# Optimization experiments

Measured on AMD Instinct MI355X. Metric: run time of the kernel, lower is better.

## Reference

```python
import jax, jax.numpy as jnp
import numpy as np

B, T, D = 64, 32, 64          # batch, timesteps, input_dim (= output_dim)
N, V, R, H = 1024, 64, 4, 512  # locations, vec_size, read/write pairs, controller_dim
DIN = D + R * V                # controller input dim


def _address(mem, k, beta, g, s, gamma, w_prev):
    # mem: [B,N,V], k: [B,V], beta/g/gamma: [B,1], s: [B,3], w_prev: [B,N]
    beta = jax.nn.softplus(beta)
    g = jax.nn.sigmoid(g)
    s = jax.nn.softmax(s, axis=1)
    gamma = 1.0 + jax.nn.softplus(gamma)
    a = mem + 1e-16
    b = k[:, None, :] + 1e-16
    na = jnp.maximum(jnp.linalg.norm(a, axis=-1), 1e-8)   # [B,N]
    nb = jnp.maximum(jnp.linalg.norm(b, axis=-1), 1e-8)   # [B,1]
    cos = jnp.sum(a * b, axis=-1) / (na * nb)             # [B,N]
    w_c = jax.nn.softmax(beta * cos, axis=1)
    w_g = g * w_c + (1.0 - g) * w_prev
    # circular shift conv, kernel width 3: out[i] = s0*w[i-1] + s1*w[i] + s2*w[i+1]
    w_s = (s[:, 0:1] * jnp.roll(w_g, 1, axis=1)
           + s[:, 1:2] * w_g
           + s[:, 2:3] * jnp.roll(w_g, -1, axis=1))
    w = w_s ** gamma
    return w / (jnp.sum(w, axis=1, keepdims=True) + 1e-16)


def _forward(x, mem_bias, lstm_h_bias, lstm_c_bias, W_ih, W_hh, b_ih, b_hh,
             read_W, read_b, write_W, write_b, read_init, out_W, out_b):
    dt = x.dtype
    mem0 = jnp.broadcast_to(mem_bias, (B, N, V)).astype(dt)
    reads0 = jnp.broadcast_to(read_init[:, None, :], (R, B, V)).astype(dt)
    h0 = jnp.broadcast_to(lstm_h_bias, (B, H)).astype(dt)
    c0 = jnp.broadcast_to(lstm_c_bias, (B, H)).astype(dt)
    ws0 = jnp.zeros((2 * R, B, N), dt)   # per-head previous weights (read_i at 2i, write_i at 2i+1)

    def step(carry, x_t):
        mem, reads, h, c, ws = carry
        contr_x = jnp.concatenate([x_t, reads.transpose(1, 0, 2).reshape(B, R * V)], axis=1)
        # single-layer LSTM cell, pytorch gate order i,f,g,o
        gates = contr_x @ W_ih.T + b_ih + h @ W_hh.T + b_hh
        gi, gf, gg, go = jnp.split(gates, 4, axis=1)
        c_new = jax.nn.sigmoid(gf) * c + jax.nn.sigmoid(gi) * jnp.tanh(gg)
        h_new = jax.nn.sigmoid(go) * jnp.tanh(c_new)
        co = h_new
        new_reads = []
        new_ws = [None] * (2 * R)
        for i in range(R):
            # read head i
            o_r = co @ read_W[i].T + read_b[i]               # [B, V+6]
            w = _address(mem, o_r[:, :V], o_r[:, V:V+1], o_r[:, V+1:V+2],
                         o_r[:, V+2:V+5], o_r[:, V+5:V+6], ws[2 * i])
            new_ws[2 * i] = w
            new_reads.append(jnp.einsum('bn,bnv->bv', w, mem))
            # write head i
            o_w = co @ write_W[i].T + write_b[i]             # [B, 3V+6]
            e = jax.nn.sigmoid(o_w[:, V+6:2*V+6])
            a = o_w[:, 2*V+6:]
            w2 = _address(mem, o_w[:, :V], o_w[:, V:V+1], o_w[:, V+1:V+2],
                          o_w[:, V+2:V+5], o_w[:, V+5:V+6], ws[2 * i + 1])
            new_ws[2 * i + 1] = w2
            mem = mem * (1.0 - w2[:, :, None] * e[:, None, :]) + w2[:, :, None] * a[:, None, :]
        final_x = jnp.concatenate([co] + new_reads, axis=1)
        y = jax.nn.sigmoid(final_x @ out_W.T + out_b)
        return (mem, jnp.stack(new_reads), h_new, c_new, jnp.stack(new_ws)), y

    _, ys = jax.lax.scan(step, (mem0, reads0, h0, c0, ws0), x.transpose(1, 0, 2))
    return ys.transpose(1, 0, 2)   # [B,T,D]


def setup_inputs() -> dict:
    key = jax.random.key(0)
    ks = jax.random.split(key, 13)
    u = lambda k, shape, s: jax.random.uniform(k, shape, jnp.float32, -s, s)
    s_mem = 1.0 / float(np.sqrt(N + V))
    s_ctl = 5.0 / float(np.sqrt(DIN + H))
    return {
        'x': jax.random.normal(ks[0], (B, T, D), jnp.float32),
        'mem_bias': u(ks[1], (N, V), s_mem),
        'lstm_h_bias': jax.random.normal(ks[2], (1, H), jnp.float32) * 0.05,
        'lstm_c_bias': jax.random.normal(ks[3], (1, H), jnp.float32) * 0.05,
        'W_ih': u(ks[4], (4 * H, DIN), s_ctl),
        'W_hh': u(ks[5], (4 * H, H), s_ctl),
        'b_ih': jnp.zeros((4 * H,), jnp.float32),
        'b_hh': jnp.zeros((4 * H,), jnp.float32),
        'read_W': u(ks[6], (R, V + 6, H), 0.05),
        'read_b': jax.random.normal(ks[7], (R, V + 6), jnp.float32) * 0.01,
        'write_W': u(ks[8], (R, 3 * V + 6, H), 0.05),
        'write_b': jax.random.normal(ks[9], (R, 3 * V + 6), jnp.float32) * 0.01,
        'read_init': jax.random.normal(ks[10], (R, V), jnp.float32) * 0.01,
        'out_W': u(ks[11], (D, H + R * V), 0.05),
        'out_b': jax.random.normal(ks[12], (D,), jnp.float32) * 0.01,
    }


def reference(x, mem_bias, lstm_h_bias, lstm_c_bias, W_ih, W_hh, b_ih, b_hh,
              read_W, read_b, write_W, write_b, read_init, out_W, out_b):
    return _forward(x, mem_bias, lstm_h_bias, lstm_c_bias, W_ih, W_hh, b_ih, b_hh,
                    read_W, read_b, write_W, write_b, read_init, out_W, out_b)
```

## Files before the change

kernel.cpp:

```cpp
#include <hip/hip_runtime.h>
#include <math.h>

#define TT 32
#define DD 64
#define NN 1024
#define VV 64
#define RR 4
#define HH 512

typedef unsigned int uint_t;
typedef unsigned short ushort_t;

__device__ __forceinline__ float sigf(float x) { return 1.0f / (1.0f + __expf(-x)); }
__device__ __forceinline__ float splus(float x) {
  return (x > 0.f) ? (x + log1pf(__expf(-x))) : log1pf(__expf(x));
}
__device__ __forceinline__ ushort_t bfr(float f) {
  uint_t u = __float_as_uint(f);
  return (ushort_t)((u + 0x7fffu + ((u >> 16) & 1u)) >> 16);
}
__device__ __forceinline__ float bflo(uint_t u) { return __uint_as_float(u << 16); }
__device__ __forceinline__ float bfhi(uint_t u) { return __uint_as_float(u & 0xffff0000u); }
__device__ __forceinline__ uint_t packbf(float a, float b) {
  return (uint_t)bfr(a) | ((uint_t)bfr(b) << 16);
}

__global__ void build_gw(const float* __restrict__ W_ih, const float* __restrict__ W_hh,
                         const float* __restrict__ out_W, uint_t* __restrict__ W2g) {
  int idx = blockIdx.x * 256 + threadIdx.x;
  if (idx >= 2112 * 416) return;
  int r = idx / 416, kp = idx - r * 416;
  float v[2];
  #pragma unroll
  for (int q = 0; q < 2; ++q) {
    int k = 2 * kp + q;
    float f;
    if (r < 2048) {
      int h = r >> 2, g = r & 3, row = g * 512 + h;
      f = (k < 320) ? W_ih[(size_t)row * 320 + k] : W_hh[(size_t)row * 512 + (k - 320)];
    } else {
      int j = r - 2048;
      if (k < 64) f = 0.f;
      else if (k < 320) f = out_W[(size_t)j * 768 + 512 + (k - 64)];
      else f = out_W[(size_t)j * 768 + (k - 320)];
    }
    v[q] = f;
  }
  W2g[idx] = packbf(v[0], v[1]);
}
__global__ void build_hw(const float* __restrict__ read_W, const float* __restrict__ write_W,
                         uint_t* __restrict__ W2h) {
  int idx = blockIdx.x * 256 + threadIdx.x;
  if (idx >= 1072 * 256) return;
  int r = idx >> 8, kp = idx & 255;
  const float* src = (r < 280) ? (read_W + (size_t)r * 512) : (write_W + (size_t)(r - 280) * 512);
  W2h[idx] = packbf(src[2 * kp], src[2 * kp + 1]);
}
__global__ void bias_kernel(const float* __restrict__ bi, const float* __restrict__ bh,
                            float* __restrict__ o) {
  int i = blockIdx.x * 256 + threadIdx.x;
  if (i < 2048) o[i] = bi[i] + bh[i];
}
__global__ void k0_init(const float* __restrict__ x, const float* __restrict__ mem_bias,
                        const float* __restrict__ h_bias, const float* __restrict__ c_bias,
                        const float* __restrict__ read_init,
                        ushort_t* __restrict__ g_mem, uint_t* __restrict__ A2,
                        float* __restrict__ g_c, float* __restrict__ g_ws) {
  const int b = blockIdx.x, tid = threadIdx.x;
  {
    const float4* src = (const float4*)(mem_bias + (size_t)tid * VV);
    uint4* dst = (uint4*)(g_mem + (size_t)b * (NN * VV) + (size_t)tid * VV);
    #pragma unroll
    for (int p = 0; p < 8; ++p) {
      float4 va = src[2 * p], vb = src[2 * p + 1];
      uint4 o;
      o.x = packbf(va.x, va.y); o.y = packbf(va.z, va.w);
      o.z = packbf(vb.x, vb.y); o.w = packbf(vb.z, vb.w);
      dst[p] = o;
    }
  }
  if (tid < 416) {
    float v0, v1;
    if (tid < 32)      { v0 = x[((size_t)b * TT) * DD + 2 * tid]; v1 = x[((size_t)b * TT) * DD + 2 * tid + 1]; }
    else if (tid < 160){ int e = 2 * (tid - 32); v0 = read_init[e]; v1 = read_init[e + 1]; }
    else               { int e = 2 * (tid - 160); v0 = h_bias[e]; v1 = h_bias[e + 1]; }
    A2[(size_t)tid * 64 + b] = packbf(v0, v1);
  }
  if (tid < 512) g_c[(size_t)tid * 64 + b] = c_bias[tid];
  for (int i = tid; i < 8192; i += 1024) g_ws[(size_t)b * 8192 + i] = 0.f;
}

__global__ __launch_bounds__(512) void k1s(
    int par, int doGate, int doOut,
    const uint_t* __restrict__ W2g, const uint_t* __restrict__ A2,
    float* __restrict__ g_gp) {
  const int blk = blockIdx.x, tid = threadIdx.x;
  const int lane = tid & 63, u = tid >> 6;
  const bool isGate = (blk < 128);
  if (isGate && !doGate) return;
  if (!isGate && !doOut) return;
  __shared__ uint_t s_tile[52 * 64];
  int kh, hglob = 0, orow = 0;
  size_t wbase;
  if (isGate) {
    int grp = blk >> 1; kh = blk & 1;
    hglob = grp * 8 + u;
    wbase = (size_t)(hglob * 4) * 416;
  } else {
    int ob = blk - 128; kh = ob & 1;
    orow = 2048 + (ob >> 1) * 8 + u;
    wbase = (size_t)orow * 416;
  }
  float acc0 = 0.f, acc1 = 0.f, acc2 = 0.f, acc3 = 0.f;
  for (int cc = 0; cc < 4; ++cc) {
    int c = kh * 4 + cc;
    for (int i = tid; i < 52 * 64; i += 512) {
      int kk = i >> 6, bb = i & 63;
      int kpg = c * 52 + kk;
      int phys = (kpg < 160) ? kpg : kpg + 256 * par;
      s_tile[i] = A2[(size_t)phys * 64 + bb];
    }
    __syncthreads();
    const uint4* w4 = (const uint4*)(W2g + wbase) + c * 13;
    if (isGate) {
      #pragma unroll
      for (int q = 0; q < 13; ++q) {
        uint4 wA = w4[q], wB = w4[104 + q], wC = w4[208 + q], wD = w4[312 + q];
        const uint_t* pA = (const uint_t*)&wA;
        const uint_t* pB = (const uint_t*)&wB;
        const uint_t* pC = (const uint_t*)&wC;
        const uint_t* pD = (const uint_t*)&wD;
        #pragma unroll
        for (int jj = 0; jj < 4; ++jj) {
          uint_t ua = s_tile[(q * 4 + jj) * 64 + lane];
          float a0 = bflo(ua), a1 = bfhi(ua);
          acc0 += bflo(pA[jj]) * a0 + bfhi(pA[jj]) * a1;
          acc1 += bflo(pB[jj]) * a0 + bfhi(pB[jj]) * a1;
          acc2 += bflo(pC[jj]) * a0 + bfhi(pC[jj]) * a1;
          acc3 += bflo(pD[jj]) * a0 + bfhi(pD[jj]) * a1;
        }
      }
    } else {
      #pragma unroll
      for (int q = 0; q < 13; ++q) {
        uint4 wA = w4[q];
        const uint_t* pA = (const uint_t*)&wA;
        #pragma unroll
        for (int jj = 0; jj < 4; ++jj) {
          uint_t ua = s_tile[(q * 4 + jj) * 64 + lane];
          acc0 += bflo(pA[jj]) * bflo(ua) + bfhi(pA[jj]) * bfhi(ua);
        }
      }
    }
    __syncthreads();
  }
  if (isGate) {
    float* d = g_gp + (size_t)(kh * 2112 + hglob * 4) * 64 + lane;
    d[0] = acc0; d[64] = acc1; d[128] = acc2; d[192] = acc3;
  } else {
    g_gp[(size_t)(kh * 2112 + orow) * 64 + lane] = acc0;
  }
}

__global__ __launch_bounds__(512) void k1c(
    int t, int par, int doGate,
    const float* __restrict__ g_gp, const float* __restrict__ gbias,
    uint_t* __restrict__ A2, float* __restrict__ g_c,
    const float* __restrict__ out_b, float* __restrict__ out) {
  const int blk = blockIdx.x, tid = threadIdx.x;
  const int lane = tid & 63, u = tid >> 6;
  if (blk < 64) {
    if (!doGate) return;
    __shared__ float s_h[512];
    const int hglob = blk * 8 + u;
    const float* p0 = g_gp + (size_t)(hglob * 4) * 64 + lane;
    const float* p1 = g_gp + (size_t)(2112 + hglob * 4) * 64 + lane;
    float gi = gbias[hglob]        + p0[0]   + p1[0];
    float gf = gbias[512 + hglob]  + p0[64]  + p1[64];
    float gg = gbias[1024 + hglob] + p0[128] + p1[128];
    float go = gbias[1536 + hglob] + p0[192] + p1[192];
    float c0 = g_c[(size_t)hglob * 64 + lane];
    float cn = sigf(gf) * c0 + sigf(gi) * tanhf(gg);
    float hn = sigf(go) * tanhf(cn);
    g_c[(size_t)hglob * 64 + lane] = cn;
    s_h[u * 64 + lane] = hn;
    __syncthreads();
    if (tid < 256) {
      int q = tid >> 6;
      float h0 = s_h[(2 * q) * 64 + lane], h1 = s_h[(2 * q + 1) * 64 + lane];
      int kp = 160 + 256 * (par ^ 1) + blk * 4 + q;
      A2[(size_t)kp * 64 + lane] = packbf(h0, h1);
    }
  } else {
    if (t == 0) return;
    int j = (blk - 64) * 8 + u;
    float v = out_b[j] + g_gp[(size_t)(2048 + j) * 64 + lane]
                       + g_gp[(size_t)(2112 + 2048 + j) * 64 + lane];
    out[((size_t)lane * TT + (t - 1)) * DD + j] = sigf(v);
  }
}

__global__ __launch_bounds__(512) void k2_heads(
    int wslot, const uint_t* __restrict__ W2h,
    const float* __restrict__ read_b, const float* __restrict__ write_b,
    const uint_t* __restrict__ A2, float* __restrict__ g_headp) {
  const int blk = blockIdx.x, tid = threadIdx.x;
  const int lane = tid & 63, u = tid >> 6;
  const int rgrp = blk >> 1, kh = blk & 1;
  const int r = rgrp * 8 + u;
  __shared__ uint_t s_tile[64 * 64];
  __shared__ float s_tr[8 * 65];
  const int hbase = 160 + 256 * wslot + kh * 128;
  float acc = 0.f;
  const uint_t* wrow = W2h + (size_t)r * 256 + kh * 128;
  for (int c = 0; c < 2; ++c) {
    for (int i = tid; i < 64 * 64; i += 512) {
      int kk = i >> 6, bb = i & 63;
      s_tile[i] = A2[(size_t)(hbase + c * 64 + kk) * 64 + bb];
    }
    __syncthreads();
    #pragma unroll 4
    for (int kk = 0; kk < 64; ++kk) {
      uint_t ua = s_tile[kk * 64 + lane];
      uint_t w = wrow[c * 64 + kk];
      acc += bflo(w) * bflo(ua) + bfhi(w) * bfhi(ua);
    }
    __syncthreads();
  }
  if (kh == 0) acc += (r < 280) ? read_b[r] : write_b[r - 280];
  s_tr[u * 65 + lane] = acc;
  __syncthreads();
  if (tid < 128) {
    int bb = tid & 63, half = tid >> 6;
    float4 v;
    v.x = s_tr[(half * 4 + 0) * 65 + bb];
    v.y = s_tr[(half * 4 + 1) * 65 + bb];
    v.z = s_tr[(half * 4 + 2) * 65 + bb];
    v.w = s_tr[(half * 4 + 3) * 65 + bb];
    *(float4*)(g_headp + (size_t)kh * 69632 + (size_t)bb * 1088 + rgrp * 8 + half * 4) = v;
  }
}

__global__ __launch_bounds__(1024, 4) void k3_mem(
    int t, const float* __restrict__ x, const float* __restrict__ g_headp,
    ushort_t* __restrict__ g_mem, uint_t* __restrict__ A2,
    float* __restrict__ g_ws) {
  const int b = blockIdx.x, tid = threadIdx.x;
  const int lane = tid & 63, wave = tid >> 6;
  extern __shared__ uint_t s_mem[];
  __shared__ alignas(16) float s_wgA[1024];
  __shared__ alignas(16) float s_wgB[1024];
  __shared__ alignas(16) float s_part[1024];
  __shared__ alignas(16) float s_reads[RR * VV];
  __shared__ alignas(16) float s_or[72];
  __shared__ alignas(16) float s_ow[200];
  __shared__ alignas(16) float s_e[VV];
  __shared__ alignas(16) float s_a[VV];
  __shared__ float s_redR[16];
  __shared__ float s_redW[16];
  uint_t* m32 = (uint_t*)(g_mem + (size_t)b * (NN * VV));
  const float* hp = g_headp + (size_t)b * 1088;
  const float* hp1 = hp + 69632;

  float wsr[8];
  #pragma unroll
  for (int s2 = 0; s2 < 8; ++s2) wsr[s2] = g_ws[(size_t)(b * 8 + s2) * 1024 + tid];

  if (tid < 70) s_or[tid] = hp[tid] + hp1[tid];
  else if (tid >= 128 && tid < 326) s_ow[tid - 128] = hp[280 + (tid - 128)] + hp1[280 + (tid - 128)];
  __syncthreads();
  if (tid < VV) { s_e[tid] = sigf(s_ow[70 + tid]); s_a[tid] = s_ow[134 + tid]; }

  for (int hd = 0; hd < RR; ++hd) {
    float dotR = 0.f, dotW = 0.f, nrm2 = 0.f;
    if (hd == 0) {
      const uint4* rowp = (const uint4*)(m32 + (size_t)tid * 32);
      const float4* orf = (const float4*)s_or;
      const float4* owf = (const float4*)s_ow;
      #pragma unroll
      for (int p = 0; p < 8; ++p) {
        uint4 m = rowp[p];
        s_mem[tid * 32 + ((4 * p + 0 + tid) & 31)] = m.x;
        s_mem[tid * 32 + ((4 * p + 1 + tid) & 31)] = m.y;
        s_mem[tid * 32 + ((4 * p + 2 + tid) & 31)] = m.z;
        s_mem[tid * 32 + ((4 * p + 3 + tid) & 31)] = m.w;
        float4 ka = orf[2 * p], kb = orf[2 * p + 1];
        float4 wa = owf[2 * p], wb = owf[2 * p + 1];
        float m0 = bflo(m.x), m1 = bfhi(m.x), m2 = bflo(m.y), m3 = bfhi(m.y);
        float m4 = bflo(m.z), m5 = bfhi(m.z), m6 = bflo(m.w), m7 = bfhi(m.w);
        nrm2 += m0 * m0 + m1 * m1 + m2 * m2 + m3 * m3 + m4 * m4 + m5 * m5 + m6 * m6 + m7 * m7;
        dotR += m0 * ka.x + m1 * ka.y + m2 * ka.z + m3 * ka.w +
                m4 * kb.x + m5 * kb.y + m6 * kb.z + m7 * kb.w;
        dotW += m0 * wa.x + m1 * wa.y + m2 * wa.z + m3 * wa.w +
                m4 * wb.x + m5 * wb.y + m6 * wb.z + m7 * wb.w;
      }
    } else {
      #pragma unroll 8
      for (int c = 0; c < 32; ++c) {
        uint_t u = s_mem[tid * 32 + ((c + tid) & 31)];
        float v0 = bflo(u), v1 = bfhi(u);
        nrm2 += v0 * v0 + v1 * v1;
        dotR += v0 * s_or[2 * c] + v1 * s_or[2 * c + 1];
        dotW += v0 * s_ow[2 * c] + v1 * s_ow[2 * c + 1];
      }
    }
    float kkR, kkW;
    {
      float kR = s_or[lane]; kR *= kR;
      float kW = s_ow[lane]; kW *= kW;
      #pragma unroll
      for (int o = 32; o; o >>= 1) { kR += __shfl_xor(kR, o); kW += __shfl_xor(kW, o); }
      kkR = kR; kkW = kW;
    }
    float na = fmaxf(sqrtf(nrm2), 1e-8f);

    float nbR = fmaxf(sqrtf(kkR), 1e-8f), nbW = fmaxf(sqrtf(kkW), 1e-8f);
    float betaR = splus(s_or[64]), betaW = splus(s_ow[64]);
    float gR = sigf(s_or[65]), gW = sigf(s_ow[65]);
    float r0 = s_or[66], r1 = s_or[67], r2 = s_or[68];
    float q0 = s_ow[66], q1 = s_ow[67], q2 = s_ow[68];
    float mxR = fmaxf(r0, fmaxf(r1, r2)), mxW = fmaxf(q0, fmaxf(q1, q2));
    float eR0 = __expf(r0 - mxR), eR1 = __expf(r1 - mxR), eR2 = __expf(r2 - mxR);
    float eW0 = __expf(q0 - mxW), eW1 = __expf(q1 - mxW), eW2 = __expf(q2 - mxW);
    float siR = 1.0f / (eR0 + eR1 + eR2), siW = 1.0f / (eW0 + eW1 + eW2);
    float gamR = 1.0f + splus(s_or[69]), gamW = 1.0f + splus(s_ow[69]);
    float eeR = __expf(betaR * dotR / (na * nbR));
    float eeW = __expf(betaW * dotW / (na * nbW));
    float vR = eeR, vW = eeW;
    #pragma unroll
    for (int o = 32; o; o >>= 1) { vR += __shfl_xor(vR, o); vW += __shfl_xor(vW, o); }
    if (lane == 0) { s_redR[wave] = vR; s_redW[wave] = vW; }
    __syncthreads();
    float SR = 0.f, SW = 0.f;
    #pragma unroll
    for (int w = 0; w < 16; ++w) { SR += s_redR[w]; SW += s_redW[w]; }
    float wgR = gR * (eeR / SR) + (1.0f - gR) * wsr[2 * hd];
    float wgW = gW * (eeW / SW) + (1.0f - gW) * wsr[2 * hd + 1];
    s_wgA[tid] = wgR;
    s_wgB[tid] = wgW;
    __syncthreads();
    int tm = (tid + 1023) & 1023, tp = (tid + 1) & 1023;
    float wsnR = (eR0 * siR) * s_wgA[tm] + (eR1 * siR) * s_wgA[tid] + (eR2 * siR) * s_wgA[tp];
    float wsnW = (eW0 * siW) * s_wgB[tm] + (eW1 * siW) * s_wgB[tid] + (eW2 * siW) * s_wgB[tp];
    float wpR = __expf(gamR * __logf(wsnR));
    float wpW = __expf(gamW * __logf(wsnW));
    vR = wpR; vW = wpW;
    #pragma unroll
    for (int o = 32; o; o >>= 1) { vR += __shfl_xor(vR, o); vW += __shfl_xor(vW, o); }
    if (lane == 0) { s_redR[wave] = vR; s_redW[wave] = vW; }
    __syncthreads();
    float ZR = 0.f, ZW = 0.f;
    #pragma unroll
    for (int w = 0; w < 16; ++w) { ZR += s_redR[w]; ZW += s_redW[w]; }
    float wRf = wpR / (ZR + 1e-16f);
    float wWf = wpW / (ZW + 1e-16f);
    s_wgA[tid] = wRf;
    s_wgB[tid] = wWf;
    g_ws[(size_t)(b * 8 + 2 * hd) * 1024 + tid] = wRf;
    g_ws[(size_t)(b * 8 + 2 * hd + 1) * 1024 + tid] = wWf;
    __syncthreads();

    if (hd < 3) {
      if (tid < 70) s_or[tid] = hp[(hd + 1) * 70 + tid] + hp1[(hd + 1) * 70 + tid];
      else if (tid >= 128 && tid < 326) {
        int i2 = tid - 128;
        s_ow[i2] = hp[280 + (hd + 1) * 198 + i2] + hp1[280 + (hd + 1) * 198 + i2];
      }
    }

    {
      const int cp = lane & 31, half = lane >> 5;
      const float e0 = s_e[2 * cp], e1 = s_e[2 * cp + 1];
      const float a0 = s_a[2 * cp], a1 = s_a[2 * cp + 1];
      const int rbase = wave * 64 + half;
      float acc0 = 0.f, acc1 = 0.f;
      #pragma unroll 8
      for (int q = 0; q < 32; ++q) {
        int row = rbase + 2 * q;
        int addr = row * 32 + ((cp + row) & 31);
        uint_t uu = s_mem[addr];
        float wRn = s_wgA[row];
        float wWn = s_wgB[row];
        float v0 = bflo(uu), v1 = bfhi(uu);
        acc0 += wRn * v0; acc1 += wRn * v1;
        float n0 = v0 * (1.f - wWn * e0) + wWn * a0;
        float n1 = v1 * (1.f - wWn * e1) + wWn * a1;
        uint_t nu = packbf(n0, n1);
        if (hd < 3) s_mem[addr] = nu;
        else        m32[(size_t)row * 32 + cp] = nu;
      }
      acc0 += __shfl_xor(acc0, 32);
      acc1 += __shfl_xor(acc1, 32);
      if (half == 0) *(float2*)(s_part + wave * 64 + 2 * cp) = make_float2(acc0, acc1);
    }
    __syncthreads();
    if (tid < VV) {
      float s = 0.f;
      #pragma unroll
      for (int w2 = 0; w2 < 16; ++w2) s += s_part[w2 * 64 + tid];
      s_reads[hd * VV + tid] = s;
      if (hd < 3) { s_e[tid] = sigf(s_ow[70 + tid]); s_a[tid] = s_ow[134 + tid]; }
    }
  }
  __syncthreads();

  if (tid < 128)
    A2[(size_t)(32 + tid) * 64 + b] = packbf(s_reads[2 * tid], s_reads[2 * tid + 1]);
  if (tid < 32 && t + 1 < TT) {
    float v0 = x[((size_t)b * TT + t + 1) * DD + 2 * tid];
    float v1 = x[((size_t)b * TT + t + 1) * DD + 2 * tid + 1];
    A2[(size_t)tid * 64 + b] = packbf(v0, v1);
  }
}

extern "C" void kernel_launch(void* const* d_in, const int* in_sizes, int n_in,
                              void* d_out, int out_size, void* d_ws, size_t ws_size,
                              hipStream_t stream) {
  char* ws = (char*)d_ws;
  ushort_t* g_mem = (ushort_t*)ws;
  uint_t* g_A2    = (uint_t*)(ws + 8388608);
  float* g_c      = (float*)(ws + 8560640);
  float* g_ws     = (float*)(ws + 8691712);
  float* g_headp  = (float*)(ws + 10788864);
  uint_t* W2g     = (uint_t*)(ws + 11345920);
  uint_t* W2h     = (uint_t*)(ws + 14860288);
  float* gbias    = (float*)(ws + 15958016);
  float* g_gp     = (float*)(ws + 15966208);

  const float* x        = (const float*)d_in[0];
  const float* mem_bias = (const float*)d_in[1];
  const float* h_bias   = (const float*)d_in[2];
  const float* c_bias   = (const float*)d_in[3];
  const float* W_ih     = (const float*)d_in[4];
  const float* W_hh     = (const float*)d_in[5];
  const float* b_ih     = (const float*)d_in[6];
  const float* b_hh     = (const float*)d_in[7];
  const float* read_W   = (const float*)d_in[8];
  const float* read_b   = (const float*)d_in[9];
  const float* write_W  = (const float*)d_in[10];
  const float* write_b  = (const float*)d_in[11];
  const float* read_init= (const float*)d_in[12];
  const float* out_W    = (const float*)d_in[13];
  const float* out_b    = (const float*)d_in[14];
  float* out = (float*)d_out;

  bias_kernel<<<8, 256, 0, stream>>>(b_ih, b_hh, gbias);
  build_gw<<<3432, 256, 0, stream>>>(W_ih, W_hh, out_W, W2g);
  build_hw<<<1072, 256, 0, stream>>>(read_W, write_W, W2h);
  k0_init<<<64, 1024, 0, stream>>>(x, mem_bias, h_bias, c_bias, read_init,
                                   g_mem, g_A2, g_c, g_ws);
  for (int t = 0; t < TT; ++t) {
    k1s<<<144, 512, 0, stream>>>(t & 1, 1, (t > 0) ? 1 : 0, W2g, g_A2, g_gp);
    k1c<<<72, 512, 0, stream>>>(t, t & 1, 1, g_gp, gbias, g_A2, g_c, out_b, out);
    k2_heads<<<268, 512, 0, stream>>>((t + 1) & 1, W2h, read_b, write_b, g_A2, g_headp);
    k3_mem<<<64, 1024, 131072, stream>>>(t, x, g_headp, g_mem, g_A2, g_ws);
  }
  k1s<<<144, 512, 0, stream>>>(0, 0, 1, W2g, g_A2, g_gp);
  k1c<<<72, 512, 0, stream>>>(TT, 0, 0, g_gp, gbias, g_A2, g_c, out_b, out);
}
```

Before: 3.883 ms.

## Split GEMV K-dimension four ways and defer weight normalization in memory kernel

The gate/output GEMV kernel and the head-projection kernel now split the reduction dimension into four slices instead of two. This doubles the block count (288 and 536 blocks) to fill more compute units on this latency-bound recurrent step, and the consumers sum four partials instead of two. The memory kernel also stores the unnormalized sharpened weights and folds 1/Z into the erase/add vectors and the read result. That removes a block-wide barrier and the normalized-weight writes to shared memory before the memory update. The cost is more partial-sum traffic, a larger workspace, and slightly different rounding from applying the normalization later.

```diff
diff --git a/kernel.cpp b/kernel.cpp
--- a/kernel.cpp
+++ b/kernel.cpp
@@ -96,24 +96,24 @@
     float* __restrict__ g_gp) {
   const int blk = blockIdx.x, tid = threadIdx.x;
   const int lane = tid & 63, u = tid >> 6;
-  const bool isGate = (blk < 128);
+  const bool isGate = (blk < 256);
   if (isGate && !doGate) return;
   if (!isGate && !doOut) return;
   __shared__ uint_t s_tile[52 * 64];
   int kh, hglob = 0, orow = 0;
   size_t wbase;
   if (isGate) {
-    int grp = blk >> 1; kh = blk & 1;
+    int grp = blk >> 2; kh = blk & 3;
     hglob = grp * 8 + u;
     wbase = (size_t)(hglob * 4) * 416;
   } else {
-    int ob = blk - 128; kh = ob & 1;
-    orow = 2048 + (ob >> 1) * 8 + u;
+    int ob = blk - 256; kh = ob & 3;
+    orow = 2048 + (ob >> 2) * 8 + u;
     wbase = (size_t)orow * 416;
   }
   float acc0 = 0.f, acc1 = 0.f, acc2 = 0.f, acc3 = 0.f;
-  for (int cc = 0; cc < 4; ++cc) {
-    int c = kh * 4 + cc;
+  for (int cc = 0; cc < 2; ++cc) {
+    int c = kh * 2 + cc;
     for (int i = tid; i < 52 * 64; i += 512) {
       int kk = i >> 6, bb = i & 63;
       int kpg = c * 52 + kk;
@@ -155,10 +155,10 @@
     __syncthreads();
   }
   if (isGate) {
-    float* d = g_gp + (size_t)(kh * 2112 + hglob * 4) * 64 + lane;
+    float* d = g_gp + (size_t)kh * 135168 + (size_t)(hglob * 4) * 64 + lane;
     d[0] = acc0; d[64] = acc1; d[128] = acc2; d[192] = acc3;
   } else {
-    g_gp[(size_t)(kh * 2112 + orow) * 64 + lane] = acc0;
+    g_gp[(size_t)kh * 135168 + (size_t)orow * 64 + lane] = acc0;
   }
 }
 
@@ -173,12 +173,13 @@
     if (!doGate) return;
     __shared__ float s_h[512];
     const int hglob = blk * 8 + u;
-    const float* p0 = g_gp + (size_t)(hglob * 4) * 64 + lane;
-    const float* p1 = g_gp + (size_t)(2112 + hglob * 4) * 64 + lane;
-    float gi = gbias[hglob]        + p0[0]   + p1[0];
-    float gf = gbias[512 + hglob]  + p0[64]  + p1[64];
-    float gg = gbias[1024 + hglob] + p0[128] + p1[128];
-    float go = gbias[1536 + hglob] + p0[192] + p1[192];
+    float gi = gbias[hglob], gf = gbias[512 + hglob];
+    float gg = gbias[1024 + hglob], go = gbias[1536 + hglob];
+    #pragma unroll
+    for (int kh = 0; kh < 4; ++kh) {
+      const float* p = g_gp + (size_t)kh * 135168 + (size_t)(hglob * 4) * 64 + lane;
+      gi += p[0]; gf += p[64]; gg += p[128]; go += p[192];
+    }
     float c0 = g_c[(size_t)hglob * 64 + lane];
     float cn = sigf(gf) * c0 + sigf(gi) * tanhf(gg);
     float hn = sigf(go) * tanhf(cn);
@@ -194,8 +195,10 @@
   } else {
     if (t == 0) return;
     int j = (blk - 64) * 8 + u;
-    float v = out_b[j] + g_gp[(size_t)(2048 + j) * 64 + lane]
-                       + g_gp[(size_t)(2112 + 2048 + j) * 64 + lane];
+    float v = out_b[j];
+    #pragma unroll
+    for (int kh = 0; kh < 4; ++kh)
+      v += g_gp[(size_t)kh * 135168 + (size_t)(2048 + j) * 64 + lane];
     out[((size_t)lane * TT + (t - 1)) * DD + j] = sigf(v);
   }
 }
@@ -206,27 +209,25 @@
     const uint_t* __restrict__ A2, float* __restrict__ g_headp) {
   const int blk = blockIdx.x, tid = threadIdx.x;
   const int lane = tid & 63, u = tid >> 6;
-  const int rgrp = blk >> 1, kh = blk & 1;
+  const int rgrp = blk >> 2, kh = blk & 3;
   const int r = rgrp * 8 + u;
   __shared__ uint_t s_tile[64 * 64];
   __shared__ float s_tr[8 * 65];
-  const int hbase = 160 + 256 * wslot + kh * 128;
+  const int hbase = 160 + 256 * wslot + kh * 64;
   float acc = 0.f;
-  const uint_t* wrow = W2h + (size_t)r * 256 + kh * 128;
-  for (int c = 0; c < 2; ++c) {
-    for (int i = tid; i < 64 * 64; i += 512) {
-      int kk = i >> 6, bb = i & 63;
-      s_tile[i] = A2[(size_t)(hbase + c * 64 + kk) * 64 + bb];
-    }
-    __syncthreads();
-    #pragma unroll 4
-    for (int kk = 0; kk < 64; ++kk) {
-      uint_t ua = s_tile[kk * 64 + lane];
-      uint_t w = wrow[c * 64 + kk];
-      acc += bflo(w) * bflo(ua) + bfhi(w) * bfhi(ua);
-    }
-    __syncthreads();
-  }
+  const uint_t* wrow = W2h + (size_t)r * 256 + kh * 64;
+  for (int i = tid; i < 64 * 64; i += 512) {
+    int kk = i >> 6, bb = i & 63;
+    s_tile[i] = A2[(size_t)(hbase + kk) * 64 + bb];
+  }
+  __syncthreads();
+  #pragma unroll 4
+  for (int kk = 0; kk < 64; ++kk) {
+    uint_t ua = s_tile[kk * 64 + lane];
+    uint_t w = wrow[kk];
+    acc += bflo(w) * bflo(ua) + bfhi(w) * bfhi(ua);
+  }
+  __syncthreads();
   if (kh == 0) acc += (r < 280) ? read_b[r] : write_b[r - 280];
   s_tr[u * 65 + lane] = acc;
   __syncthreads();
@@ -251,6 +252,7 @@
   __shared__ alignas(16) float s_wgA[1024];
   __shared__ alignas(16) float s_wgB[1024];
   __shared__ alignas(16) float s_part[1024];
+  __shared__ alignas(16) float s_wp[1024];
   __shared__ alignas(16) float s_reads[RR * VV];
   __shared__ alignas(16) float s_or[72];
   __shared__ alignas(16) float s_ow[200];
@@ -260,14 +262,23 @@
   __shared__ float s_redW[16];
   uint_t* m32 = (uint_t*)(g_mem + (size_t)b * (NN * VV));
   const float* hp = g_headp + (size_t)b * 1088;
-  const float* hp1 = hp + 69632;
 
   float wsr[8];
   #pragma unroll
   for (int s2 = 0; s2 < 8; ++s2) wsr[s2] = g_ws[(size_t)(b * 8 + s2) * 1024 + tid];
 
-  if (tid < 70) s_or[tid] = hp[tid] + hp1[tid];
-  else if (tid >= 128 && tid < 326) s_ow[tid - 128] = hp[280 + (tid - 128)] + hp1[280 + (tid - 128)];
+  if (tid < 70) {
+    float s = 0.f;
+    #pragma unroll
+    for (int kh = 0; kh < 4; ++kh) s += hp[(size_t)kh * 69632 + tid];
+    s_or[tid] = s;
+  } else if (tid >= 128 && tid < 326) {
+    int i2 = tid - 128;
+    float s = 0.f;
+    #pragma unroll
+    for (int kh = 0; kh < 4; ++kh) s += hp[(size_t)kh * 69632 + 280 + i2];
+    s_ow[i2] = s;
+  }
   __syncthreads();
   if (tid < VV) { s_e[tid] = sigf(s_ow[70 + tid]); s_a[tid] = s_ow[134 + tid]; }
 
@@ -344,6 +355,8 @@
     float wsnW = (eW0 * siW) * s_wgB[tm] + (eW1 * siW) * s_wgB[tid] + (eW2 * siW) * s_wgB[tp];
     float wpR = __expf(gamR * __logf(wsnR));
     float wpW = __expf(gamW * __logf(wsnW));
+    s_part[tid] = wpR;
+    s_wp[tid] = wpW;
     vR = wpR; vW = wpW;
     #pragma unroll
     for (int o = 32; o; o >>= 1) { vR += __shfl_xor(vR, o); vW += __shfl_xor(vW, o); }
@@ -352,26 +365,34 @@
     float ZR = 0.f, ZW = 0.f;
     #pragma unroll
     for (int w = 0; w < 16; ++w) { ZR += s_redR[w]; ZW += s_redW[w]; }
-    float wRf = wpR / (ZR + 1e-16f);
-    float wWf = wpW / (ZW + 1e-16f);
-    s_wgA[tid] = wRf;
-    s_wgB[tid] = wWf;
+    float invZR = 1.0f / (ZR + 1e-16f);
+    float invZW = 1.0f / (ZW + 1e-16f);
+    float wRf = wpR * invZR;
+    float wWf = wpW * invZW;
+    wsr[2 * hd] = wRf;
+    wsr[2 * hd + 1] = wWf;
     g_ws[(size_t)(b * 8 + 2 * hd) * 1024 + tid] = wRf;
     g_ws[(size_t)(b * 8 + 2 * hd + 1) * 1024 + tid] = wWf;
-    __syncthreads();
 
     if (hd < 3) {
-      if (tid < 70) s_or[tid] = hp[(hd + 1) * 70 + tid] + hp1[(hd + 1) * 70 + tid];
-      else if (tid >= 128 && tid < 326) {
+      if (tid < 70) {
+        float s = 0.f;
+        #pragma unroll
+        for (int kh = 0; kh < 4; ++kh) s += hp[(size_t)kh * 69632 + (hd + 1) * 70 + tid];
+        s_or[tid] = s;
+      } else if (tid >= 128 && tid < 326) {
         int i2 = tid - 128;
-        s_ow[i2] = hp[280 + (hd + 1) * 198 + i2] + hp1[280 + (hd + 1) * 198 + i2];
+        float s = 0.f;
+        #pragma unroll
+        for (int kh = 0; kh < 4; ++kh) s += hp[(size_t)kh * 69632 + 280 + (hd + 1) * 198 + i2];
+        s_ow[i2] = s;
       }
     }
 
     {
       const int cp = lane & 31, half = lane >> 5;
-      const float e0 = s_e[2 * cp], e1 = s_e[2 * cp + 1];
-      const float a0 = s_a[2 * cp], a1 = s_a[2 * cp + 1];
+      const float e0 = s_e[2 * cp] * invZW, e1 = s_e[2 * cp + 1] * invZW;
+      const float a0 = s_a[2 * cp] * invZW, a1 = s_a[2 * cp + 1] * invZW;
       const int rbase = wave * 64 + half;
       float acc0 = 0.f, acc1 = 0.f;
       #pragma unroll 8
@@ -379,8 +400,8 @@
         int row = rbase + 2 * q;
         int addr = row * 32 + ((cp + row) & 31);
         uint_t uu = s_mem[addr];
-        float wRn = s_wgA[row];
-        float wWn = s_wgB[row];
+        float wRn = s_part[row];
+        float wWn = s_wp[row];
         float v0 = bflo(uu), v1 = bfhi(uu);
         acc0 += wRn * v0; acc1 += wRn * v1;
         float n0 = v0 * (1.f - wWn * e0) + wWn * a0;
@@ -398,7 +419,7 @@
       float s = 0.f;
       #pragma unroll
       for (int w2 = 0; w2 < 16; ++w2) s += s_part[w2 * 64 + tid];
-      s_reads[hd * VV + tid] = s;
+      s_reads[hd * VV + tid] = s * invZR;
       if (hd < 3) { s_e[tid] = sigf(s_ow[70 + tid]); s_a[tid] = s_ow[134 + tid]; }
     }
   }
@@ -422,10 +443,10 @@
   float* g_c      = (float*)(ws + 8560640);
   float* g_ws     = (float*)(ws + 8691712);
   float* g_headp  = (float*)(ws + 10788864);
-  uint_t* W2g     = (uint_t*)(ws + 11345920);
-  uint_t* W2h     = (uint_t*)(ws + 14860288);
-  float* gbias    = (float*)(ws + 15958016);
-  float* g_gp     = (float*)(ws + 15966208);
+  uint_t* W2g     = (uint_t*)(ws + 11902976);
+  uint_t* W2h     = (uint_t*)(ws + 15417344);
+  float* gbias    = (float*)(ws + 16515072);
+  float* g_gp     = (float*)(ws + 16523264);
 
   const float* x        = (const float*)d_in[0];
   const float* mem_bias = (const float*)d_in[1];
@@ -450,11 +471,11 @@
   k0_init<<<64, 1024, 0, stream>>>(x, mem_bias, h_bias, c_bias, read_init,
                                    g_mem, g_A2, g_c, g_ws);
   for (int t = 0; t < TT; ++t) {
-    k1s<<<144, 512, 0, stream>>>(t & 1, 1, (t > 0) ? 1 : 0, W2g, g_A2, g_gp);
+    k1s<<<288, 512, 0, stream>>>(t & 1, 1, (t > 0) ? 1 : 0, W2g, g_A2, g_gp);
     k1c<<<72, 512, 0, stream>>>(t, t & 1, 1, g_gp, gbias, g_A2, g_c, out_b, out);
-    k2_heads<<<268, 512, 0, stream>>>((t + 1) & 1, W2h, read_b, write_b, g_A2, g_headp);
+    k2_heads<<<536, 512, 0, stream>>>((t + 1) & 1, W2h, read_b, write_b, g_A2, g_headp);
     k3_mem<<<64, 1024, 131072, stream>>>(t, x, g_headp, g_mem, g_A2, g_ws);
   }
-  k1s<<<144, 512, 0, stream>>>(0, 0, 1, W2g, g_A2, g_gp);
+  k1s<<<288, 512, 0, stream>>>(0, 0, 1, W2g, g_A2, g_gp);
   k1c<<<72, 512, 0, stream>>>(TT, 0, 0, g_gp, gbias, g_A2, g_c, out_b, out);
 }
```

New measurement: 3.278 ms. 15.6% less time.
